# Optimization experiments

Hardware: AMD Instinct MI355X
Metric: run time of the kernel (lower is better)

The kernel has to match this reference:

```python
import jax, jax.numpy as jnp
import numpy as np

B = 65536      # batch of (state, action) pairs
DIM_S = 64     # input feature dim
DIM_C = 8      # number of options / experts
H = 256        # hidden width (two hidden layers)


def setup_inputs() -> dict:
    key = jax.random.key(0)
    ks = jax.random.split(key, 7)
    s = 0.05  # small init scale
    st = jax.random.normal(ks[0], (B, DIM_S), dtype=jnp.float32)
    # Batched expert weights: one slice per expert (dim_c experts).
    W1 = jax.random.normal(ks[1], (DIM_C, DIM_S, H), dtype=jnp.float32) * s
    b1 = jax.random.normal(ks[2], (DIM_C, H), dtype=jnp.float32) * s
    W2 = jax.random.normal(ks[3], (DIM_C, H, H), dtype=jnp.float32) * s
    b2 = jax.random.normal(ks[4], (DIM_C, H), dtype=jnp.float32) * s
    W3 = jax.random.normal(ks[5], (DIM_C, H, 1), dtype=jnp.float32) * s
    b3 = jax.random.normal(ks[6], (DIM_C, 1), dtype=jnp.float32) * s
    return {"st": st, "W1": W1, "b1": b1, "W2": W2, "b2": b2,
            "W3": W3, "b3": b3}


def reference(st, W1, b1, W2, b2, W3, b3):
    # Equivalent of torch.stack([m(st) for m in self.discriminator], dim=1):
    # every expert MLP (dim_s -> H -> H -> 1, ReLU) applied to the same st,
    # expressed as batched GEMMs over the expert axis c.
    h = jax.nn.relu(jnp.einsum('bs,csh->bch', st, W1) + b1[None])   # [B, C, H]
    h = jax.nn.relu(jnp.einsum('bch,chk->bck', h, W2) + b2[None])   # [B, C, H]
    d = jnp.einsum('bch,cho->bco', h, W3) + b3[None]                # [B, C, 1]
    return d
```

## Files before the change

### kernel.cpp

```cpp
#include <hip/hip_runtime.h>
#include <hip/hip_bf16.h>

typedef __bf16 bf16x8 __attribute__((ext_vector_type(8)));
typedef float  f32x4  __attribute__((ext_vector_type(4)));

static constexpr int S  = 64;
static constexpr int C  = 8;
static constexpr int HD = 256;

__device__ __forceinline__ unsigned short f2bf(float f) {
  __hip_bfloat16 b = __float2bfloat16(f);
  unsigned short u;
  __builtin_memcpy(&u, &b, 2);
  return u;
}

__device__ __forceinline__ void gl2lds16(const void* g, void* l) {
  __builtin_amdgcn_global_load_lds(
      (const __attribute__((address_space(1))) unsigned int*)g,
      (__attribute__((address_space(3))) unsigned int*)l, 16, 0, 0);
}

__global__ __launch_bounds__(256) void prep_weights(
    const float* __restrict__ W1, const float* __restrict__ W2,
    unsigned short* __restrict__ W1T, unsigned short* __restrict__ W2T)
{
  __shared__ float tile[32][33];
  const int tid = threadIdx.x, cl = tid & 31, r0 = tid >> 5;
  const int b = blockIdx.x;
  if (b < 512) {
    const int c = b >> 6, t = b & 63, kt = t >> 3, nt = t & 7;
    const float* src = W2 + c * 65536;
    #pragma unroll
    for (int i = 0; i < 4; ++i) {
      int r = r0 + 8 * i;
      tile[r][cl] = src[(kt * 32 + r) * 256 + nt * 32 + cl];
    }
    __syncthreads();
    unsigned short* dst = W2T + c * 65536;
    #pragma unroll
    for (int i = 0; i < 4; ++i) {
      int r = r0 + 8 * i;
      dst[(nt * 32 + r) * 256 + kt * 32 + cl] = f2bf(tile[cl][r]);
    }
  } else {
    const int bb = b - 512;
    const int c = bb >> 4, t = bb & 15, st2 = t >> 3, ht = t & 7;
    const float* src = W1 + c * 16384;
    #pragma unroll
    for (int i = 0; i < 4; ++i) {
      int r = r0 + 8 * i;
      tile[r][cl] = src[(st2 * 32 + r) * 256 + ht * 32 + cl];
    }
    __syncthreads();
    unsigned short* dst = W1T + c * 16384;
    #pragma unroll
    for (int i = 0; i < 4; ++i) {
      int r = r0 + 8 * i;
      dst[(ht * 32 + r) * 64 + st2 * 32 + cl] = f2bf(tile[cl][r]);
    }
  }
}

__global__ __launch_bounds__(256, 2) void moe_fused(
    const float* __restrict__ st,
    const unsigned short* __restrict__ W1T,
    const unsigned short* __restrict__ W2T,
    const float* __restrict__ b1,
    const float* __restrict__ b2,
    const float* __restrict__ W3,
    const float* __restrict__ b3,
    float* __restrict__ out)
{
  constexpr int LDT = 72;

  __shared__ __align__(16) unsigned short sT[256 * LDT];
  __shared__ __align__(16) unsigned short sU[2 * 32 * 256];

  const int tid  = threadIdx.x;
  const int lane = tid & 63;
  const int wv   = tid >> 6;
  const int l15  = lane & 15;
  const int q    = lane >> 4;
  const int c    = blockIdx.x >> 8;
  const int row0 = (blockIdx.x & 255) * 256;

  const unsigned short* W1c = W1T + c * HD * S;
  const unsigned short* W2c = W2T + c * HD * HD;

  {
    #pragma unroll
    for (int it = 0; it < 8; ++it) {
      const int r = wv * 64 + it * 8 + (lane >> 3);
      const int g = lane & 7;
      const float4* p = reinterpret_cast<const float4*>(
          st + (size_t)(row0 + r) * S + g * 8);
      float4 x = p[0], y = p[1];
      union { uint4 u4; unsigned short us[8]; } pk;
      pk.us[0] = f2bf(x.x); pk.us[1] = f2bf(x.y); pk.us[2] = f2bf(x.z); pk.us[3] = f2bf(x.w);
      pk.us[4] = f2bf(y.x); pk.us[5] = f2bf(y.y); pk.us[6] = f2bf(y.z); pk.us[7] = f2bf(y.w);
      *reinterpret_cast<uint4*>(sU + r * 64 + ((g ^ (r & 7)) << 3)) = pk.u4;
    }
  }
  __asm__ __volatile__("s_waitcnt lgkmcnt(0)" ::: "memory");

  bf16x8 aF[4][4][2];
  #pragma unroll
  for (int cc = 0; cc < 4; ++cc) {
    f32x4 bias[4];
    #pragma unroll
    for (int mt = 0; mt < 4; ++mt)
      bias[mt] = *reinterpret_cast<const f32x4*>(
          b1 + c * HD + cc * 64 + mt * 16 + q * 4);

    f32x4 acc[4][4];
    #pragma unroll
    for (int mt = 0; mt < 4; ++mt)
      #pragma unroll
      for (int nt = 0; nt < 4; ++nt)
        acc[mt][nt] = (f32x4){0.f, 0.f, 0.f, 0.f};

    #pragma unroll
    for (int ks = 0; ks < 2; ++ks) {
      bf16x8 aW[4];
      #pragma unroll
      for (int mt = 0; mt < 4; ++mt)
        aW[mt] = *reinterpret_cast<const bf16x8*>(
            W1c + (cc * 64 + mt * 16 + l15) * S + ks * 32 + q * 8);
      bf16x8 bB[4];
      #pragma unroll
      for (int nt = 0; nt < 4; ++nt) {
        const int r = wv * 64 + nt * 16 + l15;
        const int g = ks * 4 + q;
        bB[nt] = *reinterpret_cast<const bf16x8*>(
            sU + r * 64 + ((g ^ (r & 7)) << 3));
      }
      #pragma unroll
      for (int mt = 0; mt < 4; ++mt)
        #pragma unroll
        for (int nt = 0; nt < 4; ++nt)
          acc[mt][nt] = __builtin_amdgcn_mfma_f32_16x16x32_bf16(
              aW[mt], bB[nt], acc[mt][nt], 0, 0, 0);
    }

    #pragma unroll
    for (int mt = 0; mt < 4; ++mt) {
      #pragma unroll
      for (int nt = 0; nt < 4; ++nt) {
        ushort4 pk;
        float v0 = acc[mt][nt][0] + bias[mt][0]; v0 = v0 > 0.f ? v0 : 0.f;
        float v1 = acc[mt][nt][1] + bias[mt][1]; v1 = v1 > 0.f ? v1 : 0.f;
        float v2 = acc[mt][nt][2] + bias[mt][2]; v2 = v2 > 0.f ? v2 : 0.f;
        float v3 = acc[mt][nt][3] + bias[mt][3]; v3 = v3 > 0.f ? v3 : 0.f;
        pk.x = f2bf(v0); pk.y = f2bf(v1); pk.z = f2bf(v2); pk.w = f2bf(v3);
        *reinterpret_cast<ushort4*>(
            sT + (wv * 64 + nt * 16 + l15) * LDT + mt * 16 + q * 4) = pk;
      }
    }
    __asm__ __volatile__("s_waitcnt lgkmcnt(0)" ::: "memory");
    #pragma unroll
    for (int rt = 0; rt < 4; ++rt)
      #pragma unroll
      for (int k2 = 0; k2 < 2; ++k2)
        aF[cc][rt][k2] = *reinterpret_cast<const bf16x8*>(
            sT + (wv * 64 + rt * 16 + l15) * LDT + k2 * 32 + q * 8);
    __asm__ __volatile__("s_waitcnt lgkmcnt(0)" ::: "memory");
  }

  float pb2v[8][2], pw3v[8][2];
  #pragma unroll
  for (int ch = 0; ch < 8; ++ch)
    #pragma unroll
    for (int ct = 0; ct < 2; ++ct) {
      const int n = ch * 32 + ct * 16 + l15;
      pb2v[ch][ct] = b2[c * HD + n];
      pw3v[ch][ct] = W3[c * HD + n];
    }
  const float bb3 = b3[c];

  __syncthreads();

  #pragma unroll
  for (int pc = 0; pc < 2; ++pc) {
    unsigned short* buf = sU + pc * (32 * 256);
    #pragma unroll
    for (int i = 0; i < 4; ++i) {
      const int b2i = wv * 4 + i;
      const int r   = b2i * 2 + (lane >> 5);
      const int j   = (lane & 31) ^ (r & 7);
      gl2lds16(W2c + (pc * 32 + r) * 256 + j * 8, buf + b2i * 512);
    }
  }
  __syncthreads();

  float dacc[4][4];
  #pragma unroll
  for (int rt = 0; rt < 4; ++rt)
    #pragma unroll
    for (int r = 0; r < 4; ++r) dacc[rt][r] = 0.f;

  #pragma unroll
  for (int ch = 0; ch < 8; ++ch) {
    const unsigned short* buf = sU + (ch & 1) * (32 * 256);

    f32x4 acc[4][2];
    #pragma unroll
    for (int rt = 0; rt < 4; ++rt)
      #pragma unroll
      for (int ct = 0; ct < 2; ++ct)
        acc[rt][ct] = (f32x4){0.f, 0.f, 0.f, 0.f};

    #pragma unroll
    for (int ks = 0; ks < 8; ++ks) {
      const int jj = ks * 4 + q;
      const int cc = ks >> 1, k2 = ks & 1;
      #pragma unroll
      for (int ct = 0; ct < 2; ++ct) {
        const int nl = ct * 16 + l15;
        bf16x8 b = *reinterpret_cast<const bf16x8*>(
            buf + nl * 256 + ((jj ^ (l15 & 7)) << 3));
        #pragma unroll
        for (int rt = 0; rt < 4; ++rt)
          acc[rt][ct] = __builtin_amdgcn_mfma_f32_16x16x32_bf16(
              aF[cc][rt][k2], b, acc[rt][ct], 0, 0, 0);
      }
    }

    #pragma unroll
    for (int ct = 0; ct < 2; ++ct) {
      const float bias = pb2v[ch][ct];
      const float w3v  = pw3v[ch][ct];
      #pragma unroll
      for (int rt = 0; rt < 4; ++rt)
        #pragma unroll
        for (int r = 0; r < 4; ++r) {
          float v = acc[rt][ct][r] + bias;
          v = v > 0.f ? v : 0.f;
          dacc[rt][r] += v * w3v;
        }
    }

    __syncthreads();
    if (ch < 6) {
      unsigned short* nbuf = sU + (ch & 1) * (32 * 256);
      #pragma unroll
      for (int i = 0; i < 4; ++i) {
        const int b2i = wv * 4 + i;
        const int r   = b2i * 2 + (lane >> 5);
        const int j   = (lane & 31) ^ (r & 7);
        gl2lds16(W2c + ((ch + 2) * 32 + r) * 256 + j * 8, nbuf + b2i * 512);
      }
    }
  }

  #pragma unroll
  for (int rt = 0; rt < 4; ++rt)
    #pragma unroll
    for (int r = 0; r < 4; ++r) {
      float v = dacc[rt][r];
      v += __shfl_xor(v, 1);
      v += __shfl_xor(v, 2);
      v += __shfl_xor(v, 4);
      v += __shfl_xor(v, 8);
      dacc[rt][r] = v;
    }

  if (l15 == 0) {
    const int rbase = row0 + wv * 64 + q * 4;
    #pragma unroll
    for (int rt = 0; rt < 4; ++rt)
      #pragma unroll
      for (int r = 0; r < 4; ++r)
        out[(rbase + rt * 16 + r) * C + c] = dacc[rt][r] + bb3;
  }
}

extern "C" void kernel_launch(void* const* d_in, const int* in_sizes, int n_in,
                              void* d_out, int out_size, void* d_ws, size_t ws_size,
                              hipStream_t stream)
{
  const float* st = (const float*)d_in[0];
  const float* W1 = (const float*)d_in[1];
  const float* b1 = (const float*)d_in[2];
  const float* W2 = (const float*)d_in[3];
  const float* b2 = (const float*)d_in[4];
  const float* W3 = (const float*)d_in[5];
  const float* b3 = (const float*)d_in[6];
  float* out = (float*)d_out;

  unsigned short* W1T = (unsigned short*)d_ws;
  unsigned short* W2T = W1T + C * HD * S;

  prep_weights<<<dim3(640), dim3(256), 0, stream>>>(W1, W2, W1T, W2T);
  moe_fused<<<dim3(2048), dim3(256), 0, stream>>>(st, W1T, W2T, b1, b2, W3, b3, out);
}
```

Baseline: 168.1 us.

## Keep layer-1 activations in registers and use 16x16x16 MFMA for layer 2

The layer-1 output is now packed directly from the MFMA accumulator layout into register operands for a 16x16x16 bf16 MFMA, which removes the LDS transpose round-trip through sT. With the sT buffer gone, the W2 staging chunks grow from 32 to 64 rows, so layer 2 runs 4 chunks instead of 8 with fewer barriers. The first W2 chunk prefetch is issued during the last layer-1 iteration so it overlaps compute. In exchange, the 16x16x16 MFMA does half the K per instruction, doubling the layer-2 instruction count, and the larger 4x4 accumulator tile raises register pressure.

```diff
diff --git a/kernel.cpp b/kernel.cpp
--- a/kernel.cpp
+++ b/kernel.cpp
@@ -2,6 +2,7 @@
 #include <hip/hip_bf16.h>
 
 typedef __bf16 bf16x8 __attribute__((ext_vector_type(8)));
+typedef short  s16x4  __attribute__((ext_vector_type(4)));
 typedef float  f32x4  __attribute__((ext_vector_type(4)));
 
 static constexpr int S  = 64;
@@ -72,10 +73,8 @@
     const float* __restrict__ b3,
     float* __restrict__ out)
 {
-  constexpr int LDT = 72;
-
-  __shared__ __align__(16) unsigned short sT[256 * LDT];
-  __shared__ __align__(16) unsigned short sU[2 * 32 * 256];
+  __shared__ __align__(16) unsigned short sU[64 * 256];
+  __shared__ __align__(16) unsigned short sW[64 * 256];
 
   const int tid  = threadIdx.x;
   const int lane = tid & 63;
@@ -87,24 +86,23 @@
 
   const unsigned short* W1c = W1T + c * HD * S;
   const unsigned short* W2c = W2T + c * HD * HD;
-
-  {
-    #pragma unroll
-    for (int it = 0; it < 8; ++it) {
-      const int r = wv * 64 + it * 8 + (lane >> 3);
-      const int g = lane & 7;
-      const float4* p = reinterpret_cast<const float4*>(
-          st + (size_t)(row0 + r) * S + g * 8);
-      float4 x = p[0], y = p[1];
-      union { uint4 u4; unsigned short us[8]; } pk;
-      pk.us[0] = f2bf(x.x); pk.us[1] = f2bf(x.y); pk.us[2] = f2bf(x.z); pk.us[3] = f2bf(x.w);
-      pk.us[4] = f2bf(y.x); pk.us[5] = f2bf(y.y); pk.us[6] = f2bf(y.z); pk.us[7] = f2bf(y.w);
-      *reinterpret_cast<uint4*>(sU + r * 64 + ((g ^ (r & 7)) << 3)) = pk.u4;
-    }
+  const float bb3 = b3[c];
+
+  #pragma unroll
+  for (int it = 0; it < 8; ++it) {
+    const int r = wv * 64 + it * 8 + (lane >> 3);
+    const int g = lane & 7;
+    const float4* p = reinterpret_cast<const float4*>(
+        st + (size_t)(row0 + r) * S + g * 8);
+    float4 x = p[0], y = p[1];
+    union { uint4 u4; unsigned short us[8]; } pk;
+    pk.us[0] = f2bf(x.x); pk.us[1] = f2bf(x.y); pk.us[2] = f2bf(x.z); pk.us[3] = f2bf(x.w);
+    pk.us[4] = f2bf(y.x); pk.us[5] = f2bf(y.y); pk.us[6] = f2bf(y.z); pk.us[7] = f2bf(y.w);
+    *reinterpret_cast<uint4*>(sU + r * 64 + ((g ^ (r & 7)) << 3)) = pk.u4;
   }
   __asm__ __volatile__("s_waitcnt lgkmcnt(0)" ::: "memory");
 
-  bf16x8 aF[4][4][2];
+  s16x4 aF[16][4];
   #pragma unroll
   for (int cc = 0; cc < 4; ++cc) {
     f32x4 bias[4];
@@ -143,93 +141,86 @@
               aW[mt], bB[nt], acc[mt][nt], 0, 0, 0);
     }
 
-    #pragma unroll
-    for (int mt = 0; mt < 4; ++mt) {
+    if (cc == 3) {
+      #pragma unroll
+      for (int i = 0; i < 8; ++i) {
+        const int u = wv * 8 + i;
+        const int r = u * 2 + (lane >> 5);
+        const int j = (lane & 31) ^ (r & 7);
+        gl2lds16(W2c + r * 256 + j * 8, sW + u * 512);
+      }
+    }
+
+    #pragma unroll
+    for (int mt = 0; mt < 4; ++mt)
       #pragma unroll
       for (int nt = 0; nt < 4; ++nt) {
-        ushort4 pk;
         float v0 = acc[mt][nt][0] + bias[mt][0]; v0 = v0 > 0.f ? v0 : 0.f;
         float v1 = acc[mt][nt][1] + bias[mt][1]; v1 = v1 > 0.f ? v1 : 0.f;
         float v2 = acc[mt][nt][2] + bias[mt][2]; v2 = v2 > 0.f ? v2 : 0.f;
         float v3 = acc[mt][nt][3] + bias[mt][3]; v3 = v3 > 0.f ? v3 : 0.f;
-        pk.x = f2bf(v0); pk.y = f2bf(v1); pk.z = f2bf(v2); pk.w = f2bf(v3);
-        *reinterpret_cast<ushort4*>(
-            sT + (wv * 64 + nt * 16 + l15) * LDT + mt * 16 + q * 4) = pk;
-      }
-    }
-    __asm__ __volatile__("s_waitcnt lgkmcnt(0)" ::: "memory");
+        s16x4 pk;
+        pk[0] = (short)f2bf(v0); pk[1] = (short)f2bf(v1);
+        pk[2] = (short)f2bf(v2); pk[3] = (short)f2bf(v3);
+        aF[cc * 4 + mt][nt] = pk;
+      }
+  }
+
+  __syncthreads();
+
+  #pragma unroll
+  for (int i = 0; i < 8; ++i) {
+    const int u = wv * 8 + i;
+    const int r = u * 2 + (lane >> 5);
+    const int j = (lane & 31) ^ (r & 7);
+    gl2lds16(W2c + (64 + r) * 256 + j * 8, sU + u * 512);
+  }
+  __syncthreads();
+
+  float dacc[4][4];
+  #pragma unroll
+  for (int rt = 0; rt < 4; ++rt)
+    #pragma unroll
+    for (int r = 0; r < 4; ++r) dacc[rt][r] = 0.f;
+
+  #pragma unroll
+  for (int ch = 0; ch < 4; ++ch) {
+    const unsigned short* buf = (ch & 1) ? sU : sW;
+
+    float pb2v[4], pw3v[4];
+    #pragma unroll
+    for (int ct = 0; ct < 4; ++ct) {
+      const int n = ch * 64 + ct * 16 + l15;
+      pb2v[ct] = b2[c * HD + n];
+      pw3v[ct] = W3[c * HD + n];
+    }
+
+    f32x4 acc[4][4];
     #pragma unroll
     for (int rt = 0; rt < 4; ++rt)
       #pragma unroll
-      for (int k2 = 0; k2 < 2; ++k2)
-        aF[cc][rt][k2] = *reinterpret_cast<const bf16x8*>(
-            sT + (wv * 64 + rt * 16 + l15) * LDT + k2 * 32 + q * 8);
-    __asm__ __volatile__("s_waitcnt lgkmcnt(0)" ::: "memory");
-  }
-
-  float pb2v[8][2], pw3v[8][2];
-  #pragma unroll
-  for (int ch = 0; ch < 8; ++ch)
-    #pragma unroll
-    for (int ct = 0; ct < 2; ++ct) {
-      const int n = ch * 32 + ct * 16 + l15;
-      pb2v[ch][ct] = b2[c * HD + n];
-      pw3v[ch][ct] = W3[c * HD + n];
-    }
-  const float bb3 = b3[c];
-
-  __syncthreads();
-
-  #pragma unroll
-  for (int pc = 0; pc < 2; ++pc) {
-    unsigned short* buf = sU + pc * (32 * 256);
-    #pragma unroll
-    for (int i = 0; i < 4; ++i) {
-      const int b2i = wv * 4 + i;
-      const int r   = b2i * 2 + (lane >> 5);
-      const int j   = (lane & 31) ^ (r & 7);
-      gl2lds16(W2c + (pc * 32 + r) * 256 + j * 8, buf + b2i * 512);
-    }
-  }
-  __syncthreads();
-
-  float dacc[4][4];
-  #pragma unroll
-  for (int rt = 0; rt < 4; ++rt)
-    #pragma unroll
-    for (int r = 0; r < 4; ++r) dacc[rt][r] = 0.f;
-
-  #pragma unroll
-  for (int ch = 0; ch < 8; ++ch) {
-    const unsigned short* buf = sU + (ch & 1) * (32 * 256);
-
-    f32x4 acc[4][2];
-    #pragma unroll
-    for (int rt = 0; rt < 4; ++rt)
-      #pragma unroll
-      for (int ct = 0; ct < 2; ++ct)
+      for (int ct = 0; ct < 4; ++ct)
         acc[rt][ct] = (f32x4){0.f, 0.f, 0.f, 0.f};
 
     #pragma unroll
-    for (int ks = 0; ks < 8; ++ks) {
-      const int jj = ks * 4 + q;
-      const int cc = ks >> 1, k2 = ks & 1;
-      #pragma unroll
-      for (int ct = 0; ct < 2; ++ct) {
+    for (int kk = 0; kk < 16; ++kk) {
+      #pragma unroll
+      for (int ct = 0; ct < 4; ++ct) {
         const int nl = ct * 16 + l15;
-        bf16x8 b = *reinterpret_cast<const bf16x8*>(
-            buf + nl * 256 + ((jj ^ (l15 & 7)) << 3));
+        const int p16 = (kk * 2 + (q >> 1)) ^ (nl & 7);
+        s16x4 bW = *reinterpret_cast<const s16x4*>(
+            buf + nl * 256 + p16 * 8 + (q & 1) * 4);
         #pragma unroll
         for (int rt = 0; rt < 4; ++rt)
-          acc[rt][ct] = __builtin_amdgcn_mfma_f32_16x16x32_bf16(
-              aF[cc][rt][k2], b, acc[rt][ct], 0, 0, 0);
-      }
-    }
-
-    #pragma unroll
-    for (int ct = 0; ct < 2; ++ct) {
-      const float bias = pb2v[ch][ct];
-      const float w3v  = pw3v[ch][ct];
+          acc[rt][ct] = __builtin_amdgcn_mfma_f32_16x16x16bf16_1k(
+              aF[kk][rt], bW, acc[rt][ct], 0, 0, 0);
+      }
+    }
+
+    #pragma unroll
+    for (int ct = 0; ct < 4; ++ct) {
+      const float bias = pb2v[ct];
+      const float w3v  = pw3v[ct];
       #pragma unroll
       for (int rt = 0; rt < 4; ++rt)
         #pragma unroll
@@ -240,15 +231,17 @@
         }
     }
 
-    __syncthreads();
-    if (ch < 6) {
-      unsigned short* nbuf = sU + (ch & 1) * (32 * 256);
-      #pragma unroll
-      for (int i = 0; i < 4; ++i) {
-        const int b2i = wv * 4 + i;
-        const int r   = b2i * 2 + (lane >> 5);
-        const int j   = (lane & 31) ^ (r & 7);
-        gl2lds16(W2c + ((ch + 2) * 32 + r) * 256 + j * 8, nbuf + b2i * 512);
+    if (ch < 3) {
+      __syncthreads();
+      if (ch < 2) {
+        unsigned short* nbuf = (ch & 1) ? sU : sW;
+        #pragma unroll
+        for (int i = 0; i < 8; ++i) {
+          const int u = wv * 8 + i;
+          const int r = u * 2 + (lane >> 5);
+          const int j = (lane & 31) ^ (r & 7);
+          gl2lds16(W2c + ((ch + 2) * 64 + r) * 256 + j * 8, nbuf + u * 512);
+        }
       }
     }
   }
```

Result: slower. 232.0 us (+38.0%).
